# Kernel optimization log

Hardware: AMD Instinct MI355X
Metric: run time of the kernel (lower is better)

Reference implementation:

```python
import jax, jax.numpy as jnp
import numpy as np

N = 50000      # total nodes across batched graphs
E = 400000     # directed edges (before self-loops)
B = 256        # number of graphs / protein embeddings
F_IN = 78      # atom features (num_features_xd)
H1, F1 = 10, 78   # gcn1: heads=10, out=78 -> concat 780
F2 = 128       # gcn2 output_dim (heads=1)
EMB = 320      # PLM embed_dim
PLM = 128      # plm_layers[0]
BN_EPS = 1e-5


def setup_inputs() -> dict:
    key = jax.random.key(0)
    ks = jax.random.split(key, 30)
    g = lambda k, s, sc=0.05: (jax.random.normal(k, s, jnp.float32) * sc)
    inp = {
        'x': jax.random.normal(ks[0], (N, F_IN), jnp.float32),
        'edge_index': jax.random.randint(ks[1], (2, E), 0, N),
        # deterministic sorted assignment guarantees every graph id in [0,B) is populated
        'batch': (jnp.arange(N) * B) // N,
        'target_embedding': jax.random.normal(ks[2], (B, EMB), jnp.float32),
        # GATConv 1 (78 -> 78, heads=10, concat)
        'W1': g(ks[3], (F_IN, H1 * F1)), 'a1s': g(ks[4], (H1, F1)), 'a1d': g(ks[5], (H1, F1)), 'b1': g(ks[6], (H1 * F1,)),
        # GATConv 2 (780 -> 128, heads=1)
        'W2': g(ks[7], (H1 * F1, F2)), 'a2s': g(ks[8], (1, F2)), 'a2d': g(ks[9], (1, F2)), 'b2': g(ks[10], (F2,)),
        # fc_g1
        'Wg': g(ks[11], (F2, F2)), 'bg': g(ks[12], (F2,)),
        # PLM branch: Linear(320,128) + BatchNorm1d(128) in eval mode
        'Wxt': g(ks[13], (EMB, PLM)), 'bxt': g(ks[14], (PLM,)),
        'gamma': jnp.ones((PLM,), jnp.float32), 'beta': jnp.zeros((PLM,), jnp.float32),
        'rmean': g(ks[15], (PLM,)), 'rvar': jax.random.uniform(ks[16], (PLM,), jnp.float32, 0.5, 1.5),
        # head MLP
        'Wf1': g(ks[17], (F2 + PLM, 1024)), 'bf1': g(ks[18], (1024,)),
        'Wf2': g(ks[19], (1024, 256)), 'bf2': g(ks[20], (256,)),
        'Wo': g(ks[21], (256, 1)), 'bo': g(ks[22], (1,)),
    }
    return inp


def gat_conv(x, src, dst, W, a_s, a_d, b, n):
    """PyG-style GATConv (self-loops already included in src/dst)."""
    H, F = a_s.shape
    h = (x @ W).reshape(-1, H, F)                        # [n, H, F]
    e = jax.nn.leaky_relu((h * a_s).sum(-1)[src] + (h * a_d).sum(-1)[dst], 0.2)  # [e, H]
    m = jax.ops.segment_max(e, dst, num_segments=n)      # segment softmax over incoming edges
    p = jnp.exp(e - m[dst])
    denom = jax.ops.segment_sum(p, dst, num_segments=n)
    alpha = p / denom[dst]                               # [e, H]
    out = jax.ops.segment_sum(alpha[:, :, None] * h[src], dst, num_segments=n)  # [n, H, F]
    return out.reshape(-1, H * F) + b


def reference(x, edge_index, batch, target_embedding, W1, a1s, a1d, b1, W2, a2s, a2d, b2,
              Wg, bg, Wxt, bxt, gamma, beta, rmean, rvar, Wf1, bf1, Wf2, bf2, Wo, bo):
    n = x.shape[0]
    loop = jnp.arange(n)
    src = jnp.concatenate([edge_index[0], loop])   # add self-loops (GATConv default)
    dst = jnp.concatenate([edge_index[1], loop])
    h = jax.nn.elu(gat_conv(x, src, dst, W1, a1s, a1d, b1, n))      # [N, 780]
    h = jax.nn.relu(gat_conv(h, src, dst, W2, a2s, a2d, b2, n))     # [N, 128]
    g = jax.ops.segment_max(h, batch, num_segments=B)               # global max pool [B, 128]
    g = jax.nn.relu(g @ Wg + bg)
    xt = target_embedding @ Wxt + bxt
    xt = jax.nn.relu((xt - rmean) / jnp.sqrt(rvar + BN_EPS) * gamma + beta)  # BN eval
    xc = jnp.concatenate([g, xt], axis=1)                           # [B, 256]
    xc = jax.nn.relu(xc @ Wf1 + bf1)
    xc = jax.nn.relu(xc @ Wf2 + bf2)
    return xc @ Wo + bo                                             # [B, 1]
```

## Files before the change

### kernel.cpp

```cpp
#include <hip/hip_runtime.h>
#include <hip/hip_fp16.h>
#include <math.h>

static constexpr int F2 = 128, EMB = 320;

typedef _Float16 h8v __attribute__((ext_vector_type(8)));
typedef float f4v __attribute__((ext_vector_type(4)));

union F4H2 { float4 f; __half2 h[4]; };
union F2H2 { float2 f; __half2 h[2]; };

__device__ __forceinline__ __half2 shfl_xor_h2(__half2 v, int off) {
    union { __half2 h; float f; } u;
    u.h = v;
    u.f = __shfl_xor(u.f, off);
    return u.h;
}

__device__ __forceinline__ void esd(const int* src, const int* dst, int E, int e, int& s, int& d) {
    if (e < E) { s = src[e]; d = dst[e]; }
    else       { s = e - E; d = s; }
}

__global__ void k_count(const int* __restrict__ src, const int* __restrict__ dst, int E, int Etot,
                        int* __restrict__ cnt) {
    int e = blockIdx.x * 256 + threadIdx.x;
    if (e >= Etot) return;
    int s, d;
    esd(src, dst, E, e, s, d);
    atomicAdd(&cnt[d], 1);
}

__global__ void k_scan1(const int* __restrict__ in, int* __restrict__ out, int* __restrict__ bsum,
                        int n) {
    __shared__ int tmp[256];
    int t = threadIdx.x;
    int gid = blockIdx.x * 256 + t;
    int v = gid < n ? in[gid] : 0;
    tmp[t] = v;
    __syncthreads();
    for (int off = 1; off < 256; off <<= 1) {
        int u = (t >= off) ? tmp[t - off] : 0;
        __syncthreads();
        tmp[t] += u;
        __syncthreads();
    }
    if (gid < n) out[gid] = tmp[t] - v;
    if (t == 255) bsum[blockIdx.x] = tmp[255];
}

__global__ void k_scan2(int* __restrict__ bsum, int nb) {
    __shared__ int tmp[256];
    __shared__ int carry;
    int t = threadIdx.x;
    if (t == 0) carry = 0;
    __syncthreads();
    for (int base = 0; base < nb; base += 256) {
        int i = base + t;
        int v = (i < nb) ? bsum[i] : 0;
        tmp[t] = v;
        __syncthreads();
        for (int off = 1; off < 256; off <<= 1) {
            int u = (t >= off) ? tmp[t - off] : 0;
            __syncthreads();
            tmp[t] += u;
            __syncthreads();
        }
        if (i < nb) bsum[i] = tmp[t] - v + carry;
        __syncthreads();
        if (t == 0) carry += tmp[255];
        __syncthreads();
    }
}

__global__ void k_scan3(int* __restrict__ out, const int* __restrict__ bsum, int n, int Etot,
                        int* __restrict__ rp_last, int* __restrict__ cur) {
    int gid = blockIdx.x * 256 + threadIdx.x;
    if (gid < n) {
        int v = out[gid] + bsum[blockIdx.x];
        out[gid] = v;
        cur[gid] = v;
    }
    if (gid == 0) rp_last[0] = Etot;
}

__global__ void k_scatter(const int* __restrict__ src, const int* __restrict__ dst, int E, int Etot,
                          int* __restrict__ cur, int* __restrict__ csrc) {
    int e = blockIdx.x * 256 + threadIdx.x;
    if (e >= Etot) return;
    int s, d;
    esd(src, dst, E, e, s, d);
    int pos = atomicAdd(&cur[d], 1);
    csrc[pos] = s;
}

__global__ void k_prep_w(const float* __restrict__ W1, const float* __restrict__ a1s,
                         const float* __restrict__ a1d, const float* __restrict__ W2,
                         __half* __restrict__ W1T, float* __restrict__ wes,
                         float* __restrict__ wed, __half* __restrict__ W2T) {
    int idx = blockIdx.x * 256 + threadIdx.x;
    if (idx < 76800) {
        int h = idx / (80 * 96), r = idx % (80 * 96), c = r / 96, k = r % 96;
        float v = (c < 78 && k < 78) ? W1[(size_t)k * 780 + h * 78 + c] : 0.f;
        W1T[idx] = __float2half(v);
    } else if (idx < 77600) {
        int j = idx - 76800;
        int h = j / 80, k = j % 80;
        float s = 0.f, d = 0.f;
        if (k < 78) {
            for (int f = 0; f < 78; f++) {
                float w = W1[(size_t)k * 780 + h * 78 + f];
                s = fmaf(w, a1s[h * 78 + f], s);
                d = fmaf(w, a1d[h * 78 + f], d);
            }
        }
        wes[j] = s;
        wed[j] = d;
    } else if (idx < 77600 + 128 * 800) {
        int j = idx - 77600;
        int c = j / 800, k = j % 800;
        float v = (k < 780) ? W2[(size_t)k * 128 + c] : 0.f;
        W2T[j] = __float2half(v);
    }
}

__global__ void k_prep_xpk(const float* __restrict__ x, __half2* __restrict__ xpk, int N) {
    int idx = blockIdx.x * 256 + threadIdx.x;
    if (idx >= N * 64) return;
    int n = idx >> 6, l = idx & 63;
    float lo = x[(size_t)n * 78 + l];
    float hi = (64 + l < 78) ? x[(size_t)n * 78 + 64 + l] : 0.f;
    xpk[idx] = __floats2half2_rn(lo, hi);
}

__global__ void k_coefx(const float* __restrict__ x, const float* __restrict__ wes,
                        const float* __restrict__ wed, float* __restrict__ esg,
                        float* __restrict__ edg, int N) {
    int n = blockIdx.x * 256 + threadIdx.x;
    if (n >= N) return;
    float es[10] = {}, ed[10] = {};
    const float* xr = x + (size_t)n * 78;
    for (int k = 0; k < 78; k++) {
        float xv = xr[k];
#pragma unroll
        for (int h = 0; h < 10; h++) {
            es[h] = fmaf(xv, wes[h * 80 + k], es[h]);
            ed[h] = fmaf(xv, wed[h * 80 + k], ed[h]);
        }
    }
#pragma unroll
    for (int h = 0; h < 10; h++) {
        esg[(size_t)n * 16 + h] = es[h];
        edg[(size_t)n * 16 + h] = ed[h];
    }
}

__global__ void k_gatx10(const int* __restrict__ rp, const int* __restrict__ csrc,
                         const float* __restrict__ esg, const float* __restrict__ edg,
                         const __half2* __restrict__ xpk, __half* __restrict__ xagg, int N) {
    __shared__ __align__(16) __half2 pl[4][64][12];
    __shared__ __align__(16) int sl[4][64];
    int w = threadIdx.x >> 6, lane = threadIdx.x & 63;
    int node = blockIdx.x * 4 + w;
    if (node >= N) return;
    int beg = rp[node], end = rp[node + 1];
    int deg = end - beg;

    float edn[10];
    {
        const float* ep = edg + (size_t)node * 16;
        float4 a = *(const float4*)ep, b = *(const float4*)(ep + 4);
        float2 c = *(const float2*)(ep + 8);
        edn[0] = a.x; edn[1] = a.y; edn[2] = a.z; edn[3] = a.w;
        edn[4] = b.x; edn[5] = b.y; edn[6] = b.z; edn[7] = b.w;
        edn[8] = c.x; edn[9] = c.y;
    }

    __half2 acc[10];
#pragma unroll
    for (int h = 0; h < 10; h++) acc[h] = __floats2half2_rn(0.f, 0.f);

#define PASSC_BODY(LIMIT)                                                          \
    for (int i0 = 0; i0 < (LIMIT); i0 += 4) {                                      \
        int4 s4 = *(const int4*)&sl[w][i0];                                        \
        __half2 xr0 = xpk[(size_t)s4.x * 64 + lane];                               \
        __half2 xr1 = xpk[(size_t)s4.y * 64 + lane];                               \
        __half2 xr2 = xpk[(size_t)s4.z * 64 + lane];                               \
        __half2 xr3 = xpk[(size_t)s4.w * 64 + lane];                               \
        _Pragma("unroll")                                                          \
        for (int j = 0; j < 4; j++) {                                              \
            F4H2 qa, qb; F2H2 qc;                                                  \
            qa.f = *(const float4*)&pl[w][i0 + j][0];                              \
            qb.f = *(const float4*)&pl[w][i0 + j][4];                              \
            qc.f = *(const float2*)&pl[w][i0 + j][8];                              \
            __half2 xr = (j == 0) ? xr0 : (j == 1) ? xr1 : (j == 2) ? xr2 : xr3;   \
            acc[0] = __hfma2(qa.h[0], xr, acc[0]);                                 \
            acc[1] = __hfma2(qa.h[1], xr, acc[1]);                                 \
            acc[2] = __hfma2(qa.h[2], xr, acc[2]);                                 \
            acc[3] = __hfma2(qa.h[3], xr, acc[3]);                                 \
            acc[4] = __hfma2(qb.h[0], xr, acc[4]);                                 \
            acc[5] = __hfma2(qb.h[1], xr, acc[5]);                                 \
            acc[6] = __hfma2(qb.h[2], xr, acc[6]);                                 \
            acc[7] = __hfma2(qb.h[3], xr, acc[7]);                                 \
            acc[8] = __hfma2(qc.h[0], xr, acc[8]);                                 \
            acc[9] = __hfma2(qc.h[1], xr, acc[9]);                                 \
        }                                                                          \
    }

#define STASH(PVEC)                                                                \
    {                                                                              \
        F4H2 wa, wb; F2H2 wc;                                                      \
        _Pragma("unroll")                                                          \
        for (int h = 0; h < 4; h++) wa.h[h] = __float2half2_rn(PVEC[h]);           \
        _Pragma("unroll")                                                          \
        for (int h = 0; h < 4; h++) wb.h[h] = __float2half2_rn(PVEC[4 + h]);       \
        wc.h[0] = __float2half2_rn(PVEC[8]);                                       \
        wc.h[1] = __float2half2_rn(PVEC[9]);                                       \
        *(float4*)&pl[w][lane][0] = wa.f;                                          \
        *(float4*)&pl[w][lane][4] = wb.f;                                          \
        *(float2*)&pl[w][lane][8] = wc.f;                                          \
        sl[w][lane] = s;                                                           \
    }

    if (deg <= 64) {
        bool act = lane < deg;
        int s = act ? csrc[beg + lane] : 0;
        float p[10];
        if (act) {
            const float* sp = esg + (size_t)s * 16;
            float4 a = *(const float4*)sp, b = *(const float4*)(sp + 4);
            float2 c = *(const float2*)(sp + 8);
            float v[10];
            v[0] = a.x + edn[0]; v[1] = a.y + edn[1]; v[2] = a.z + edn[2]; v[3] = a.w + edn[3];
            v[4] = b.x + edn[4]; v[5] = b.y + edn[5]; v[6] = b.z + edn[6]; v[7] = b.w + edn[7];
            v[8] = c.x + edn[8]; v[9] = c.y + edn[9];
#pragma unroll
            for (int h = 0; h < 10; h++) {
                float vv = v[h] >= 0.f ? v[h] : 0.2f * v[h];
                p[h] = __expf(vv);
            }
        } else {
#pragma unroll
            for (int h = 0; h < 10; h++) p[h] = 0.f;
        }
        __half2 sh[5];
#pragma unroll
        for (int j = 0; j < 5; j++) sh[j] = __floats2half2_rn(p[2 * j], p[2 * j + 1]);
        int start = (deg <= 16) ? 8 : 32;
        for (int off = start; off; off >>= 1) {
#pragma unroll
            for (int j = 0; j < 5; j++) sh[j] = __hadd2(sh[j], shfl_xor_h2(sh[j], off));
        }
#pragma unroll
        for (int j = 0; j < 5; j++) {
            float2 f = __half22float2(sh[j]);
            p[2 * j] *= 1.f / f.x;
            p[2 * j + 1] *= 1.f / f.y;
        }
        STASH(p)
        PASSC_BODY(deg)
    } else {
        float ssf[10] = {};
        for (int cb = beg; cb < end; cb += 64) {
            int e = cb + lane;
            bool act = e < end;
            int si = act ? csrc[e] : 0;
            if (act) {
                const float* sp = esg + (size_t)si * 16;
#pragma unroll
                for (int h = 0; h < 10; h++) {
                    float vv = sp[h] + edn[h];
                    vv = vv >= 0.f ? vv : 0.2f * vv;
                    ssf[h] += __expf(vv);
                }
            }
        }
#pragma unroll
        for (int off = 32; off; off >>= 1) {
#pragma unroll
            for (int h = 0; h < 10; h++) ssf[h] += __shfl_xor(ssf[h], off);
        }
        float inv[10];
#pragma unroll
        for (int h = 0; h < 10; h++) inv[h] = 1.f / ssf[h];

        for (int cb = beg; cb < end; cb += 64) {
            int cnt = min(64, end - cb);
            int e = cb + lane;
            bool act = e < end;
            int s = act ? csrc[e] : 0;
            float p[10];
            if (act) {
                const float* sp = esg + (size_t)s * 16;
#pragma unroll
                for (int h = 0; h < 10; h++) {
                    float vv = sp[h] + edn[h];
                    vv = vv >= 0.f ? vv : 0.2f * vv;
                    p[h] = __expf(vv) * inv[h];
                }
            } else {
#pragma unroll
                for (int h = 0; h < 10; h++) p[h] = 0.f;
            }
            STASH(p)
            PASSC_BODY(cnt)
        }
    }
#undef PASSC_BODY
#undef STASH

    __half* op = xagg + (size_t)node * 800;
#pragma unroll
    for (int h = 0; h < 10; h++) {
        __half* hp = op + h * 80;
        hp[lane] = __low2half(acc[h]);
        if (lane < 16) hp[64 + lane] = __high2half(acc[h]);
    }
}

__global__ __launch_bounds__(256) void k_gemmQ(const __half* __restrict__ xagg,
                                               const __half* __restrict__ W1T,
                                               const float* __restrict__ b1,
                                               const __half* __restrict__ W2T,
                                               const float* __restrict__ a2s,
                                               const float* __restrict__ a2d,
                                               __half* __restrict__ h216,
                                               float* __restrict__ es2,
                                               float* __restrict__ ed2, int N) {
    constexpr int LQ = 808;
    __shared__ __align__(16) _Float16 qlds[16 * LQ];
    __shared__ float sered[4][2][16];
    int w = threadIdx.x >> 6, lane = threadIdx.x & 63;
    int row0 = blockIdx.x * 16;
    int col16 = lane & 15, grp = lane >> 4;
    int ko = grp * 8;
    int rbase = grp * 4;
    int ar = min(row0 + col16, N - 1);

    for (int i = threadIdx.x; i < 16 * 28; i += 256) {
        int r = i / 28, c = 780 + i % 28;
        qlds[r * LQ + c] = (_Float16)0.f;
    }

    const _Float16* Ab = (const _Float16*)xagg + (size_t)ar * 800 + ko;
    int h0 = (w < 2) ? w * 3 : 6 + (w - 2) * 2;
    int nh = (w < 2) ? 3 : 2;
    for (int hh = 0; hh < nh; hh++) {
        int h = h0 + hh;
        f4v acc1[5] = {};
        const _Float16* Ap = Ab + h * 80;
        const _Float16* Bp = (const _Float16*)W1T + ((size_t)h * 80 + col16) * 96 + ko;
#pragma unroll
        for (int ks = 0; ks < 3; ks++) {
            h8v a = *(const h8v*)(Ap + ks * 32);
#pragma unroll
            for (int t = 0; t < 5; t++) {
                h8v b = *(const h8v*)(Bp + (size_t)t * 16 * 96 + ks * 32);
                acc1[t] = __builtin_amdgcn_mfma_f32_16x16x32_f16(a, b, acc1[t], 0, 0, 0);
            }
        }
#pragma unroll
        for (int t = 0; t < 5; t++) {
            int c = t * 16 + col16;
            if (c < 78) {
                float bias = b1[h * 78 + c];
#pragma unroll
                for (int r = 0; r < 4; r++) {
                    float v = acc1[t][r] + bias;
                    float e = v > 0.f ? v : (__expf(v) - 1.f);
                    qlds[(rbase + r) * LQ + h * 78 + c] = (_Float16)e;
                }
            }
        }
    }
    __syncthreads();

    f4v acc[2] = {};
    const _Float16* Bq = (const _Float16*)W2T + (size_t)col16 * 800 + ko;
    const _Float16* Aq = qlds + (size_t)col16 * LQ + ko;
    for (int ks = 0; ks < 25; ks++) {
        h8v a = *(const h8v*)(Aq + ks * 32);
#pragma unroll
        for (int t = 0; t < 2; t++) {
            h8v b = *(const h8v*)(Bq + (size_t)(w * 2 + t) * 16 * 800 + ks * 32);
            acc[t] = __builtin_amdgcn_mfma_f32_16x16x32_f16(a, b, acc[t], 0, 0, 0);
        }
    }
    float wa[2], wb[2];
#pragma unroll
    for (int t = 0; t < 2; t++) {
        wa[t] = a2s[(w * 2 + t) * 16 + col16];
        wb[t] = a2d[(w * 2 + t) * 16 + col16];
    }
#pragma unroll
    for (int r = 0; r < 4; r++) {
        int n = row0 + rbase + r;
        float se = 0.f, sd = 0.f;
#pragma unroll
        for (int t = 0; t < 2; t++) {
            float v = acc[t][r];
            se = fmaf(v, wa[t], se);
            sd = fmaf(v, wb[t], sd);
            if (n < N) h216[(size_t)n * 128 + (w * 2 + t) * 16 + col16] = __float2half(v);
        }
#pragma unroll
        for (int off = 1; off < 16; off <<= 1) {
            se += __shfl_xor(se, off);
            sd += __shfl_xor(sd, off);
        }
        if (col16 == 0) {
            sered[w][0][rbase + r] = se;
            sered[w][1][rbase + r] = sd;
        }
    }
    __syncthreads();
    if (threadIdx.x < 16) {
        int n = row0 + threadIdx.x;
        if (n < N) {
            es2[n] = sered[0][0][threadIdx.x] + sered[1][0][threadIdx.x] +
                     sered[2][0][threadIdx.x] + sered[3][0][threadIdx.x];
            ed2[n] = sered[0][1][threadIdx.x] + sered[1][1][threadIdx.x] +
                     sered[2][1][threadIdx.x] + sered[3][1][threadIdx.x];
        }
    }
}

__global__ void k_gatP(const int* __restrict__ rp, const int* __restrict__ csrc,
                       const float* __restrict__ es, const float* __restrict__ ed,
                       const __half2* __restrict__ h216, const float* __restrict__ b2,
                       const int* __restrict__ batch, unsigned* __restrict__ gb, int N) {
    __shared__ float red[4][128];
    __shared__ int bids[4];
    __shared__ __align__(16) __half2 plP[4][64];
    __shared__ __align__(16) int slP[4][64];
    int w = threadIdx.x >> 6, lane = threadIdx.x & 63;
    int node = blockIdx.x * 4 + w;
    bool valid = node < N;

    __half2 acc = __floats2half2_rn(0.f, 0.f);
    int bid = -1;

#define PASSC2(LIMIT)                                                      \
    for (int i0 = 0; i0 < (LIMIT); i0 += 4) {                              \
        int4 s4 = *(const int4*)&slP[w][i0];                               \
        F4H2 q; q.f = *(const float4*)&plP[w][i0];                         \
        __half2 f0 = h216[(size_t)s4.x * 64 + lane];                       \
        __half2 f1 = h216[(size_t)s4.y * 64 + lane];                       \
        __half2 f2 = h216[(size_t)s4.z * 64 + lane];                       \
        __half2 f3 = h216[(size_t)s4.w * 64 + lane];                       \
        acc = __hfma2(q.h[0], f0, acc);                                    \
        acc = __hfma2(q.h[1], f1, acc);                                    \
        acc = __hfma2(q.h[2], f2, acc);                                    \
        acc = __hfma2(q.h[3], f3, acc);                                    \
    }

    if (valid) {
        int beg = rp[node], end = rp[node + 1];
        int deg = end - beg;
        float edn = ed[node];
        bid = batch[node];

        if (deg <= 64) {
            bool act = lane < deg;
            int s = act ? csrc[beg + lane] : 0;
            float p = 0.f;
            if (act) {
                float v = es[s] + edn;
                v = v >= 0.f ? v : 0.2f * v;
                p = __expf(v);
            }
            float ss = p;
            int start = (deg <= 16) ? 8 : 32;
            for (int off = start; off; off >>= 1) ss += __shfl_xor(ss, off);
            p *= 1.f / ss;
            plP[w][lane] = __float2half2_rn(p);
            slP[w][lane] = s;
            PASSC2(deg)
        } else {
            float ss = 0.f;
            for (int cb = beg; cb < end; cb += 64) {
                int e = cb + lane;
                bool act = e < end;
                int s = act ? csrc[e] : 0;
                if (act) {
                    float v = es[s] + edn;
                    v = v >= 0.f ? v : 0.2f * v;
                    ss += __expf(v);
                }
            }
#pragma unroll
            for (int off = 32; off; off >>= 1) ss += __shfl_xor(ss, off);
            float inv = 1.f / ss;
            for (int cb = beg; cb < end; cb += 64) {
                int cnt = min(64, end - cb);
                int e = cb + lane;
                bool act = e < end;
                int s = act ? csrc[e] : 0;
                float p = 0.f;
                if (act) {
                    float v = es[s] + edn;
                    v = v >= 0.f ? v : 0.2f * v;
                    p = __expf(v) * inv;
                }
                plP[w][lane] = __float2half2_rn(p);
                slP[w][lane] = s;
                PASSC2(cnt)
            }
        }
    }
#undef PASSC2

    float2 af = __half22float2(acc);
    red[w][2 * lane]     = valid ? fmaxf(af.x + b2[2 * lane], 0.f) : 0.f;
    red[w][2 * lane + 1] = valid ? fmaxf(af.y + b2[2 * lane + 1], 0.f) : 0.f;
    if (lane == 0) bids[w] = valid ? bid : -1;
    __syncthreads();
    if (threadIdx.x < 128) {
        int c = threadIdx.x;
        int b0 = bids[0];
        bool same = (bids[1] == b0) && (bids[2] == b0) && (bids[3] == b0);
        if (same && b0 >= 0) {
            float m = fmaxf(fmaxf(red[0][c], red[1][c]), fmaxf(red[2][c], red[3][c]));
            atomicMax(&gb[(size_t)b0 * 128 + c], __float_as_uint(m));
        } else {
#pragma unroll
            for (int w2 = 0; w2 < 4; w2++) {
                if (bids[w2] >= 0)
                    atomicMax(&gb[(size_t)bids[w2] * 128 + c], __float_as_uint(red[w2][c]));
            }
        }
    }
}

__global__ void k_head_gxt(const unsigned* __restrict__ gbits, const float* __restrict__ Wg,
                           const float* __restrict__ bg, const float* __restrict__ te,
                           const float* __restrict__ Wxt, const float* __restrict__ bxt,
                           const float* __restrict__ gamma, const float* __restrict__ beta,
                           const float* __restrict__ rmean, const float* __restrict__ rvar,
                           float* __restrict__ xc) {
    __shared__ float sg[F2];
    __shared__ float st[EMB];
    int b = blockIdx.x, t = threadIdx.x;
    if (t < 128) {
        sg[t] = __uint_as_float(gbits[(size_t)b * F2 + t]);
    } else {
        for (int k = t - 128; k < EMB; k += 128) st[k] = te[(size_t)b * EMB + k];
    }
    __syncthreads();
    if (t < 128) {
        float acc = bg[t];
        for (int k = 0; k < F2; k++) acc = fmaf(sg[k], Wg[k * F2 + t], acc);
        xc[(size_t)b * 256 + t] = fmaxf(acc, 0.f);
    } else {
        int c = t - 128;
        float acc = bxt[c];
        for (int k = 0; k < EMB; k++) acc = fmaf(st[k], Wxt[k * F2 + c], acc);
        acc = (acc - rmean[c]) * rsqrtf(rvar[c] + 1e-5f) * gamma[c] + beta[c];
        xc[(size_t)b * 256 + 128 + c] = fmaxf(acc, 0.f);
    }
}

__global__ void k_head_mlp(const float* __restrict__ xc, const float* __restrict__ Wf1,
                           const float* __restrict__ bf1, const float* __restrict__ Wf2,
                           const float* __restrict__ bf2, const float* __restrict__ Wo,
                           const float* __restrict__ bo, float* __restrict__ out) {
    __shared__ float s0[256];
    __shared__ float s1[1024];
    int b = blockIdx.x, t = threadIdx.x;
    s0[t] = xc[(size_t)b * 256 + t];
    __syncthreads();
    for (int col = t; col < 1024; col += 256) {
        float acc = bf1[col];
        for (int k = 0; k < 256; k++) acc = fmaf(s0[k], Wf1[k * 1024 + col], acc);
        s1[col] = fmaxf(acc, 0.f);
    }
    __syncthreads();
    {
        float acc = bf2[t];
        for (int k = 0; k < 1024; k++) acc = fmaf(s1[k], Wf2[k * 256 + t], acc);
        float v = fmaxf(acc, 0.f);
        __syncthreads();
        s0[t] = v * Wo[t];
    }
    __syncthreads();
    if (t < 64) {
        float acc = s0[t] + s0[64 + t] + s0[128 + t] + s0[192 + t];
        for (int off = 32; off; off >>= 1) acc += __shfl_down(acc, off);
        if (t == 0) out[b] = acc + bo[0];
    }
}

extern "C" void kernel_launch(void* const* d_in, const int* in_sizes, int n_in,
                              void* d_out, int out_size, void* d_ws, size_t ws_size,
                              hipStream_t stream) {
    const float* x     = (const float*)d_in[0];
    const int*   ei    = (const int*)d_in[1];
    const int*   batch = (const int*)d_in[2];
    const float* te    = (const float*)d_in[3];
    const float* W1    = (const float*)d_in[4];
    const float* a1s   = (const float*)d_in[5];
    const float* a1d   = (const float*)d_in[6];
    const float* b1    = (const float*)d_in[7];
    const float* W2    = (const float*)d_in[8];
    const float* a2s   = (const float*)d_in[9];
    const float* a2d   = (const float*)d_in[10];
    const float* b2    = (const float*)d_in[11];
    const float* Wg    = (const float*)d_in[12];
    const float* bg    = (const float*)d_in[13];
    const float* Wxt   = (const float*)d_in[14];
    const float* bxt   = (const float*)d_in[15];
    const float* gamma = (const float*)d_in[16];
    const float* beta  = (const float*)d_in[17];
    const float* rmean = (const float*)d_in[18];
    const float* rvar  = (const float*)d_in[19];
    const float* Wf1   = (const float*)d_in[20];
    const float* bf1   = (const float*)d_in[21];
    const float* Wf2   = (const float*)d_in[22];
    const float* bf2   = (const float*)d_in[23];
    const float* Wo    = (const float*)d_in[24];
    const float* bo    = (const float*)d_in[25];

    const int N = in_sizes[0] / 78;
    const int E = in_sizes[1] / 2;
    const int B = in_sizes[3] / EMB;
    const int Etot = E + N;
    const int* src = ei;
    const int* dst = ei + E;

    char* p = (char*)d_ws;
    auto alloc = [&](size_t bytes) -> void* {
        void* r = p;
        p += (bytes + 255) & ~(size_t)255;
        return r;
    };
    __half2*  xpk  = (__half2*)alloc((size_t)N * 64 * 4);
    __half*   xagg = (__half*)alloc((size_t)N * 800 * 2 + 256);
    __half*   h216 = (__half*)alloc((size_t)N * 128 * 2);
    float*    esg  = (float*)alloc((size_t)N * 16 * 4);
    float*    edg  = (float*)alloc((size_t)N * 16 * 4);
    float*    es2  = (float*)alloc((size_t)N * 4);
    float*    ed2  = (float*)alloc((size_t)N * 4);
    __half*   W1T  = (__half*)alloc((size_t)10 * 80 * 96 * 2);
    __half*   W2T  = (__half*)alloc((size_t)128 * 800 * 2);
    float*    wes  = (float*)alloc((size_t)800 * 4);
    float*    wed  = (float*)alloc((size_t)800 * 4);
    int*      cnt  = (int*)alloc((size_t)N * 4);
    int*      rp   = (int*)alloc((size_t)(N + 1) * 4);
    int*      cur  = (int*)alloc((size_t)N * 4);
    int*      csrc = (int*)alloc((size_t)Etot * 4);
    int*      bsum = (int*)alloc((size_t)1024 * 4);
    unsigned* gb   = (unsigned*)alloc((size_t)B * F2 * 4);
    float*    xc   = (float*)alloc((size_t)B * 256 * 4);

    auto gsz = [](long long t) { return (int)((t + 255) / 256); };
    const int nb = gsz(N);
    const int nwave = (N + 3) / 4;
    const int nrow16 = (N + 15) / 16;

    hipMemsetAsync(cnt, 0, (size_t)N * 4, stream);
    k_count<<<gsz(Etot), 256, 0, stream>>>(src, dst, E, Etot, cnt);
    k_scan1<<<nb, 256, 0, stream>>>(cnt, rp, bsum, N);
    k_scan2<<<1, 256, 0, stream>>>(bsum, nb);
    k_scan3<<<nb, 256, 0, stream>>>(rp, bsum, N, Etot, rp + N, cur);
    k_scatter<<<gsz(Etot), 256, 0, stream>>>(src, dst, E, Etot, cur, csrc);

    k_prep_w<<<gsz(77600 + 128 * 800), 256, 0, stream>>>(W1, a1s, a1d, W2, W1T, wes, wed, W2T);
    k_prep_xpk<<<gsz((long long)N * 64), 256, 0, stream>>>(x, xpk, N);
    k_coefx<<<nb, 256, 0, stream>>>(x, wes, wed, esg, edg, N);
    hipMemsetAsync(gb, 0, (size_t)B * F2 * 4, stream);

    k_gatx10<<<nwave, 256, 0, stream>>>(rp, csrc, esg, edg, xpk, xagg, N);

    k_gemmQ<<<nrow16, 256, 0, stream>>>(xagg, W1T, b1, W2T, a2s, a2d, h216, es2, ed2, N);

    k_gatP<<<nwave, 256, 0, stream>>>(rp, csrc, es2, ed2, (const __half2*)h216, b2, batch, gb, N);

    k_head_gxt<<<B, 256, 0, stream>>>(gb, Wg, bg, te, Wxt, bxt, gamma, beta, rmean, rvar, xc);
    k_head_mlp<<<B, 256, 0, stream>>>(xc, Wf1, bf1, Wf2, bf2, Wo, bo, (float*)d_out);
}
```

Measured before the change: 328.8 us.

## Split gemmQ hidden dimension into two chunks to halve LDS footprint

The fused GEMM kernel now processes the 780-wide intermediate in two halves of five heads (390 columns, padded to 416). Each half goes through the ELU into a smaller shared buffer and is immediately reduced into the second GEMM's accumulators. W2 is re-laid out into two padded chunks to match. Halving the LDS buffer should allow more resident blocks per CU, at the cost of an extra barrier pair and poorer wave balance, since one wave gets two heads per chunk while the others get one.

Result: slower. 358.4 us (+9.0%).

```diff
diff --git a/kernel.cpp b/kernel.cpp
--- a/kernel.cpp
+++ b/kernel.cpp
@@ -97,7 +97,7 @@
 __global__ void k_prep_w(const float* __restrict__ W1, const float* __restrict__ a1s,
                          const float* __restrict__ a1d, const float* __restrict__ W2,
                          __half* __restrict__ W1T, float* __restrict__ wes,
-                         float* __restrict__ wed, __half* __restrict__ W2T) {
+                         float* __restrict__ wed, __half* __restrict__ W2c) {
     int idx = blockIdx.x * 256 + threadIdx.x;
     if (idx < 76800) {
         int h = idx / (80 * 96), r = idx % (80 * 96), c = r / 96, k = r % 96;
@@ -116,11 +116,11 @@
         }
         wes[j] = s;
         wed[j] = d;
-    } else if (idx < 77600 + 128 * 800) {
+    } else if (idx < 77600 + 128 * 832) {
         int j = idx - 77600;
-        int c = j / 800, k = j % 800;
-        float v = (k < 780) ? W2[(size_t)k * 128 + c] : 0.f;
-        W2T[j] = __float2half(v);
+        int c = j / 832, r = j % 832, ch = r / 416, k = r % 416;
+        float v = (k < 390) ? W2[(size_t)(ch * 390 + k) * 128 + c] : 0.f;
+        W2c[j] = __float2half(v);
     }
 }
 
@@ -321,13 +321,13 @@
 __global__ __launch_bounds__(256) void k_gemmQ(const __half* __restrict__ xagg,
                                                const __half* __restrict__ W1T,
                                                const float* __restrict__ b1,
-                                               const __half* __restrict__ W2T,
+                                               const __half* __restrict__ W2c,
                                                const float* __restrict__ a2s,
                                                const float* __restrict__ a2d,
                                                __half* __restrict__ h216,
                                                float* __restrict__ es2,
                                                float* __restrict__ ed2, int N) {
-    constexpr int LQ = 808;
+    constexpr int LQ = 416;
     __shared__ __align__(16) _Float16 qlds[16 * LQ];
     __shared__ float sered[4][2][16];
     int w = threadIdx.x >> 6, lane = threadIdx.x & 63;
@@ -337,55 +337,59 @@
     int rbase = grp * 4;
     int ar = min(row0 + col16, N - 1);
 
-    for (int i = threadIdx.x; i < 16 * 28; i += 256) {
-        int r = i / 28, c = 780 + i % 28;
+    for (int i = threadIdx.x; i < 16 * 26; i += 256) {
+        int r = i / 26, c = 390 + i % 26;
         qlds[r * LQ + c] = (_Float16)0.f;
     }
 
     const _Float16* Ab = (const _Float16*)xagg + (size_t)ar * 800 + ko;
-    int h0 = (w < 2) ? w * 3 : 6 + (w - 2) * 2;
-    int nh = (w < 2) ? 3 : 2;
-    for (int hh = 0; hh < nh; hh++) {
-        int h = h0 + hh;
-        f4v acc1[5] = {};
-        const _Float16* Ap = Ab + h * 80;
-        const _Float16* Bp = (const _Float16*)W1T + ((size_t)h * 80 + col16) * 96 + ko;
-#pragma unroll
-        for (int ks = 0; ks < 3; ks++) {
-            h8v a = *(const h8v*)(Ap + ks * 32);
+    const _Float16* Aq = qlds + (size_t)col16 * LQ + ko;
+    f4v acc[2] = {};
+
+#pragma unroll
+    for (int ch = 0; ch < 2; ch++) {
+        for (int hh = w; hh < 5; hh += 4) {
+            int h = ch * 5 + hh;
+            f4v acc1[5] = {};
+            const _Float16* Ap = Ab + h * 80;
+            const _Float16* Bp = (const _Float16*)W1T + ((size_t)h * 80 + col16) * 96 + ko;
+#pragma unroll
+            for (int ks = 0; ks < 3; ks++) {
+                h8v a = *(const h8v*)(Ap + ks * 32);
+#pragma unroll
+                for (int t = 0; t < 5; t++) {
+                    h8v b = *(const h8v*)(Bp + (size_t)t * 16 * 96 + ks * 32);
+                    acc1[t] = __builtin_amdgcn_mfma_f32_16x16x32_f16(a, b, acc1[t], 0, 0, 0);
+                }
+            }
 #pragma unroll
             for (int t = 0; t < 5; t++) {
-                h8v b = *(const h8v*)(Bp + (size_t)t * 16 * 96 + ks * 32);
-                acc1[t] = __builtin_amdgcn_mfma_f32_16x16x32_f16(a, b, acc1[t], 0, 0, 0);
-            }
-        }
-#pragma unroll
-        for (int t = 0; t < 5; t++) {
-            int c = t * 16 + col16;
-            if (c < 78) {
-                float bias = b1[h * 78 + c];
-#pragma unroll
-                for (int r = 0; r < 4; r++) {
-                    float v = acc1[t][r] + bias;
-                    float e = v > 0.f ? v : (__expf(v) - 1.f);
-                    qlds[(rbase + r) * LQ + h * 78 + c] = (_Float16)e;
+                int c = t * 16 + col16;
+                if (c < 78) {
+                    float bias = b1[h * 78 + c];
+#pragma unroll
+                    for (int r = 0; r < 4; r++) {
+                        float v = acc1[t][r] + bias;
+                        float e = v > 0.f ? v : (__expf(v) - 1.f);
+                        qlds[(rbase + r) * LQ + hh * 78 + c] = (_Float16)e;
+                    }
                 }
             }
         }
-    }
-    __syncthreads();
-
-    f4v acc[2] = {};
-    const _Float16* Bq = (const _Float16*)W2T + (size_t)col16 * 800 + ko;
-    const _Float16* Aq = qlds + (size_t)col16 * LQ + ko;
-    for (int ks = 0; ks < 25; ks++) {
-        h8v a = *(const h8v*)(Aq + ks * 32);
-#pragma unroll
-        for (int t = 0; t < 2; t++) {
-            h8v b = *(const h8v*)(Bq + (size_t)(w * 2 + t) * 16 * 800 + ks * 32);
-            acc[t] = __builtin_amdgcn_mfma_f32_16x16x32_f16(a, b, acc[t], 0, 0, 0);
-        }
-    }
+        __syncthreads();
+        const _Float16* Bq = (const _Float16*)W2c + ((size_t)(w * 2) * 16 + col16) * 832 +
+                             ch * 416 + ko;
+        for (int ks = 0; ks < 13; ks++) {
+            h8v a = *(const h8v*)(Aq + ks * 32);
+#pragma unroll
+            for (int t = 0; t < 2; t++) {
+                h8v b = *(const h8v*)(Bq + (size_t)t * 16 * 832 + ks * 32);
+                acc[t] = __builtin_amdgcn_mfma_f32_16x16x32_f16(a, b, acc[t], 0, 0, 0);
+            }
+        }
+        __syncthreads();
+    }
+
     float wa[2], wb[2];
 #pragma unroll
     for (int t = 0; t < 2; t++) {
@@ -641,7 +645,7 @@
     float*    es2  = (float*)alloc((size_t)N * 4);
     float*    ed2  = (float*)alloc((size_t)N * 4);
     __half*   W1T  = (__half*)alloc((size_t)10 * 80 * 96 * 2);
-    __half*   W2T  = (__half*)alloc((size_t)128 * 800 * 2);
+    __half*   W2c  = (__half*)alloc((size_t)128 * 832 * 2);
     float*    wes  = (float*)alloc((size_t)800 * 4);
     float*    wed  = (float*)alloc((size_t)800 * 4);
     int*      cnt  = (int*)alloc((size_t)N * 4);
@@ -664,14 +668,14 @@
     k_scan3<<<nb, 256, 0, stream>>>(rp, bsum, N, Etot, rp + N, cur);
     k_scatter<<<gsz(Etot), 256, 0, stream>>>(src, dst, E, Etot, cur, csrc);
 
-    k_prep_w<<<gsz(77600 + 128 * 800), 256, 0, stream>>>(W1, a1s, a1d, W2, W1T, wes, wed, W2T);
+    k_prep_w<<<gsz(77600 + 128 * 832), 256, 0, stream>>>(W1, a1s, a1d, W2, W1T, wes, wed, W2c);
     k_prep_xpk<<<gsz((long long)N * 64), 256, 0, stream>>>(x, xpk, N);
     k_coefx<<<nb, 256, 0, stream>>>(x, wes, wed, esg, edg, N);
     hipMemsetAsync(gb, 0, (size_t)B * F2 * 4, stream);
 
     k_gatx10<<<nwave, 256, 0, stream>>>(rp, csrc, esg, edg, xpk, xagg, N);
 
-    k_gemmQ<<<nrow16, 256, 0, stream>>>(xagg, W1T, b1, W2T, a2s, a2d, h216, es2, ed2, N);
+    k_gemmQ<<<nrow16, 256, 0, stream>>>(xagg, W1T, b1, W2c, a2s, a2d, h216, es2, ed2, N);
 
     k_gatP<<<nwave, 256, 0, stream>>>(rp, csrc, es2, ed2, (const __half2*)h216, b2, batch, gb, N);
 
```
